# Kernel tuning notes

Hardware: AMD Instinct MI355X
Metric: run time of the kernel (lower is better)

## Reference

```python
import jax, jax.numpy as jnp
import numpy as np

N, E, IN_DIM, H, D = 100000, 1600000, 128, 4, 32


def setup_inputs() -> dict:
    key = jax.random.key(0)
    ks = jax.random.split(key, 8)
    glorot = lambda k, shape: jax.random.uniform(
        k, shape, jnp.float32, -1.0, 1.0) * np.sqrt(6.0 / (shape[0] + shape[1]))
    return {
        "x": jax.random.normal(ks[0], (N, IN_DIM), jnp.float32),
        "row": jax.random.randint(ks[1], (E,), 0, N, jnp.int32),
        "col": jax.random.randint(ks[2], (E,), 0, N, jnp.int32),
        "W_l": glorot(ks[3], (IN_DIM, H * D)),
        "W_r": glorot(ks[4], (IN_DIM, H * D)),
        "a1w": glorot(ks[5], (IN_DIM, H)),
        "a2w": glorot(ks[6], (IN_DIM, H)),
        "bias": jnp.zeros((H * D,), jnp.float32),
    }


def reference(x, row, col, W_l, W_r, a1w, a2w, bias):
    n = x.shape[0]  # num_nodes (= graph[0].max()+1 with dense random rows)
    x_l = (x @ W_l).reshape(n, H, D)          # [N,H,D]
    x_r = x @ W_r                              # [N,H*D]
    # per-edge attention logits: a1[row] + a2[col], leaky-relu(0.2)
    attn = jax.nn.leaky_relu((x @ a1w)[row] + (x @ a2w)[col], 0.2)  # [E,H]
    # segment softmax over destination rows (numerically stable)
    m = jax.ops.segment_max(attn, row, num_segments=n)               # [N,H]
    e = jnp.exp(attn - m[row])
    s = jax.ops.segment_sum(e, row, num_segments=n)                  # [N,H]
    attn_d = e / s[row]                                              # [E,H]
    # per-head SpMM: scatter-add weighted source features to destinations
    msgs = attn_d[:, :, None] * x_l[col]                             # [E,H,D]
    out = jax.ops.segment_sum(msgs, row, num_segments=n).reshape(n, H * D)
    return out + x_r + bias
```

## Files before the change

### kernel.cpp

```cpp
#include <hip/hip_runtime.h>


typedef short bfvec8 __attribute__((ext_vector_type(8)));
typedef float f32x4  __attribute__((ext_vector_type(4)));

#define BK 128
#define CAPC 3584
#define EPB 2048
#define REC 256
#define BSTR 16

__device__ __forceinline__ unsigned short f2bf(float f) {
  union { float f; unsigned int i; } v; v.f = f;
  unsigned int r = v.i + 0x7fffu + ((v.i >> 16) & 1u);
  return (unsigned short)(r >> 16);
}

__global__ __launch_bounds__(128) void wprep_k(
    const float* __restrict__ Wl, const float* __restrict__ Wr,
    const float* __restrict__ a1w, const float* __restrict__ a2w,
    unsigned short* __restrict__ Wtg, int* __restrict__ bcur, int NBK)
{
  const int n = blockIdx.x;
  const int y = blockIdx.y;
  const int k = threadIdx.x;
  if (y == 0 && n < 8) {
    int b = n * 128 + k;
    if (b < NBK) bcur[b * BSTR] = b * CAPC;
  }
  const float* W = y ? Wr : Wl;
  const float LOG2E = 1.4426950408889634f;
  float v;
  if (n < 128)      v = W[(size_t)k * 128 + n];
  else if (y)       v = 0.f;
  else if (n < 132) v = a1w[k * 4 + (n - 128)] * LOG2E;
  else              v = a2w[k * 4 + (n - 132)] * LOG2E;
  Wtg[((size_t)y * 136 + n) * 128 + k] = f2bf(v);
}

__global__ __launch_bounds__(256) void gemm_bin_k(
    const float* __restrict__ x, const unsigned short* __restrict__ Wtg,
    const float* __restrict__ bias,
    char* __restrict__ xls, float* __restrict__ out,
    float* __restrict__ s1, float* __restrict__ s2, int N,
    const int* __restrict__ row, const int* __restrict__ col,
    int* __restrict__ bcur, unsigned int* __restrict__ binned,
    int E, int NBK, int binBlocks, int gemmBlocks)
{
  __shared__ int h[1024];
  __shared__ int base[1024];
  const int bid = blockIdx.x;
  const int t = threadIdx.x;
  const bool isbin = (bid % 3 == 0) && (bid / 3 < binBlocks);

  if (isbin) {
    const int sub = bid / 3;
    const int e0 = sub * EPB;
    const int e1 = min(e0 + EPB, E);

    int rloc[8];
    for (int i = t; i < NBK; i += 256) h[i] = 0;
    __syncthreads();
    #pragma unroll
    for (int k = 0; k < 8; ++k) {
      int e = e0 + t + (k << 8);
      rloc[k] = (e < e1) ? row[e] : -1;
      if (rloc[k] >= 0) atomicAdd(&h[rloc[k] >> 7], 1);
    }
    __syncthreads();
    for (int i = t; i < NBK; i += 256) {
      int c = h[i];
      base[i] = c ? atomicAdd(&bcur[i * BSTR], c) : 0;
    }
    __syncthreads();
    for (int i = t; i < NBK; i += 256) h[i] = 0;
    __syncthreads();
    #pragma unroll
    for (int k = 0; k < 8; ++k) {
      int e = e0 + t + (k << 8);
      if (e < e1) {
        int r = rloc[k];
        unsigned c = (unsigned)col[e];
        int b = r >> 7;
        int rk = atomicAdd(&h[b], 1);
        binned[base[b] + rk] = ((unsigned)(r & 127) << 17) | c;
      }
    }
    return;
  }

  const int sub = bid - min(bid / 3 + 1, binBlocks);
  if (sub >= gemmBlocks) return;
  const int n0 = sub * 64;

  const int w    = t >> 6;
  const int lane = t & 63;
  const int m    = lane & 15;
  const int quad = lane >> 4;
  const int nrow = n0 + 16 * w + m;
  const int kb   = quad * 8;

  bfvec8 afx[4];
  #pragma unroll
  for (int kc4 = 0; kc4 < 4; ++kc4) {
    f32x4 u = (f32x4){0.f, 0.f, 0.f, 0.f};
    f32x4 v = (f32x4){0.f, 0.f, 0.f, 0.f};
    if (nrow < N) {
      const float* xp = &x[(size_t)nrow * 128 + kc4 * 32 + kb];
      u = *(const f32x4*)xp;
      v = *(const f32x4*)(xp + 4);
    }
    bfvec8 a;
    a[0] = (short)f2bf(u[0]); a[1] = (short)f2bf(u[1]);
    a[2] = (short)f2bf(u[2]); a[3] = (short)f2bf(u[3]);
    a[4] = (short)f2bf(v[0]); a[5] = (short)f2bf(v[1]);
    a[6] = (short)f2bf(v[2]); a[7] = (short)f2bf(v[3]);
    afx[kc4] = a;
  }

  const int arow = 128 + (m < 8 ? m : 7);

  #pragma unroll
  for (int y = 0; y < 2; ++y) {
    const unsigned short* Wt = Wtg + (size_t)y * 136 * 128;

    f32x4 acc[9];
    #pragma unroll
    for (int i = 0; i < 9; ++i) acc[i] = (f32x4){0.f, 0.f, 0.f, 0.f};

    #pragma unroll
    for (int kc4 = 0; kc4 < 4; ++kc4) {
      const int kc = kc4 * 32 + kb;
      #pragma unroll
      for (int nt = 0; nt < 8; ++nt) {
        bfvec8 bfr = *(const bfvec8*)&Wt[(size_t)(nt * 16 + m) * 128 + kc];
        acc[nt] = __builtin_amdgcn_mfma_f32_16x16x32_bf16(bfr, afx[kc4], acc[nt], 0, 0, 0);
      }
      if (y == 0) {
        bfvec8 ar = *(const bfvec8*)&Wt[(size_t)arow * 128 + kc];
        acc[8] = __builtin_amdgcn_mfma_f32_16x16x32_bf16(ar, afx[kc4], acc[8], 0, 0, 0);
      }
    }

    if (nrow < N) {
      if (y) {
        #pragma unroll
        for (int nt = 0; nt < 8; ++nt) {
          int c = nt * 16 + quad * 4;
          float4 b4 = *(const float4*)&bias[c];
          float4 v = make_float4(acc[nt][0] + b4.x, acc[nt][1] + b4.y,
                                 acc[nt][2] + b4.z, acc[nt][3] + b4.w);
          *(float4*)&out[(size_t)nrow * 128 + c] = v;
        }
      } else {
        #pragma unroll
        for (int nt = 0; nt < 8; ++nt) {
          int c = nt * 16 + quad * 4;
          unsigned lo = (unsigned)f2bf(acc[nt][0]) | ((unsigned)f2bf(acc[nt][1]) << 16);
          unsigned hi = (unsigned)f2bf(acc[nt][2]) | ((unsigned)f2bf(acc[nt][3]) << 16);
          *(uint2*)(xls + ((size_t)nrow << 8) + 2 * c) = make_uint2(lo, hi);
        }
        if (quad == 0) *(f32x4*)&s1[nrow * 4] = acc[8];
        else if (quad == 1) *(f32x4*)&s2[nrow * 4] = acc[8];
      }
    }
  }
}

__global__ __launch_bounds__(256) void csr_k(const unsigned int* __restrict__ binned,
    const int* __restrict__ bcur, int* __restrict__ offs, int* __restrict__ deg,
    unsigned int* __restrict__ colsort, int N)
{
  __shared__ unsigned ecache[CAPC];
  __shared__ int h[BK];
  __shared__ int sh[BK];
  const int t = threadIdx.x;
  const int b = blockIdx.x;
  const int lo = b * BK;
  const int e0 = b * CAPC;
  const int e1 = bcur[b * BSTR];

  if (t < BK) h[t] = 0;
  __syncthreads();
  for (int i = e0 + t; i < e1; i += 256) {
    unsigned p = binned[i];
    ecache[i - e0] = p;
    atomicAdd(&h[p >> 17], 1);
  }
  __syncthreads();

  int v = 0;
  if (t < BK) { v = h[t]; sh[t] = v; }
  __syncthreads();
  for (int off = 1; off < BK; off <<= 1) {
    int tv = (t < BK && t >= off) ? sh[t - off] : 0;
    __syncthreads();
    if (t < BK) sh[t] += tv;
    __syncthreads();
  }
  if (t < BK) {
    int ex = sh[t] - v;
    int node = lo + t;
    if (node < N) { offs[node] = e0 + ex; deg[node] = v; }
    h[t] = ex;
  }
  __syncthreads();
  const int cnt = e1 - e0;
  for (int i = t; i < cnt; i += 256) {
    unsigned p = ecache[i];
    int rlo = p >> 17;
    unsigned c = p & 0x1FFFFu;
    int pos = atomicAdd(&h[rlo], 1);
    colsort[e0 + pos] = c << 8;
  }
}

__global__ __launch_bounds__(256) void agg_k(const int* __restrict__ offs,
    const int* __restrict__ deg, const unsigned int* __restrict__ colsort,
    const float* __restrict__ s1, const float* __restrict__ s2,
    const char* __restrict__ xls, float* __restrict__ out, int N)
{
  const int lane = threadIdx.x & 63;
  const int n = blockIdx.x * 4 + (threadIdx.x >> 6);
  if (n >= N) return;
  const int e0 = offs[n], e1 = e0 + deg[n];
  const int h  = lane >> 4;
  const int hp = lane & 3;
  const int jj = (lane >> 2) & 7;
  const float s1c = s1[n * 4 + hp];
  const unsigned lane4 = (unsigned)(lane << 2);
  const unsigned hp4   = (unsigned)(hp << 2);
  const char* s2b = (const char*)s2;

  float acc0 = 0.f, acc1 = 0.f, wsum = 0.f;
  int i0 = e0;
  for (; i0 + 8 <= e1; i0 += 8) {
    unsigned csl = colsort[i0 + jj];
    float z2 = *(const float*)(s2b + ((csl >> 4) + hp4));
    float z = s1c + z2;
    z = fmaxf(z, 0.2f * z);
    float wv = exp2f(z);

    unsigned cs[8];
    #pragma unroll
    for (int j = 0; j < 8; ++j) cs[j] = colsort[i0 + j];
    unsigned pv[8];
    #pragma unroll
    for (int j = 0; j < 8; ++j)
      pv[j] = *(const unsigned*)(xls + (cs[j] + lane4));

    #pragma unroll
    for (int j = 0; j < 8; ++j) {
      float wj = __shfl(wv, (j << 2) | h);
      wsum += wj;
      union { unsigned u; float f; } lo, hi;
      lo.u = pv[j] << 16;
      hi.u = pv[j] & 0xffff0000u;
      acc0 += wj * lo.f;
      acc1 += wj * hi.f;
    }
  }
  if (i0 < e1) {
    const int rem = e1 - i0;
    unsigned csl = colsort[i0 + (jj < rem ? jj : rem - 1)];
    float z2 = *(const float*)(s2b + ((csl >> 4) + hp4));
    float z = s1c + z2;
    z = fmaxf(z, 0.2f * z);
    float wv = (jj < rem) ? exp2f(z) : 0.f;

    unsigned cs[8];
    #pragma unroll
    for (int j = 0; j < 8; ++j) cs[j] = colsort[i0 + (j < rem ? j : rem - 1)];
    unsigned pv[8];
    #pragma unroll
    for (int j = 0; j < 8; ++j)
      pv[j] = *(const unsigned*)(xls + (cs[j] + lane4));

    #pragma unroll
    for (int j = 0; j < 8; ++j) {
      float wj = __shfl(wv, (j << 2) | h);
      wsum += wj;
      union { unsigned u; float f; } lo, hi;
      lo.u = pv[j] << 16;
      hi.u = pv[j] & 0xffff0000u;
      acc0 += wj * lo.f;
      acc1 += wj * hi.f;
    }
  }

  float inv = (wsum > 0.f) ? (1.0f / wsum) : 0.f;
  const size_t o = (size_t)n * 128 + 2 * lane;
  float2 xr = *(const float2*)&out[o];
  float2 res; res.x = acc0 * inv + xr.x; res.y = acc1 * inv + xr.y;
  *(float2*)&out[o] = res;
}

extern "C" void kernel_launch(void* const* d_in, const int* in_sizes, int n_in,
                              void* d_out, int out_size, void* d_ws, size_t ws_size,
                              hipStream_t stream) {
  const float* x    = (const float*)d_in[0];
  const int*   row  = (const int*)d_in[1];
  const int*   col  = (const int*)d_in[2];
  const float* Wl   = (const float*)d_in[3];
  const float* Wr   = (const float*)d_in[4];
  const float* a1w  = (const float*)d_in[5];
  const float* a2w  = (const float*)d_in[6];
  const float* bias = (const float*)d_in[7];
  float* out = (float*)d_out;
  const int N = in_sizes[0] / 128;
  const int E = in_sizes[1];
  (void)n_in; (void)out_size; (void)ws_size;

  const int NBK = (N + BK - 1) / BK;

  char* ws = (char*)d_ws;
  size_t off = 0;
  auto carve = [&](size_t bytes) { void* p = ws + off; off += (bytes + 255) & ~(size_t)255; return p; };
  char* xls            = (char*)carve((size_t)N * REC);
  float* s1            = (float*)carve((size_t)N * 4 * 4);
  float* s2            = (float*)carve((size_t)N * 4 * 4);
  int* offs            = (int*)carve((size_t)N * 4);
  int* deg             = (int*)carve((size_t)N * 4);
  unsigned int* colsort= (unsigned int*)carve((size_t)NBK * CAPC * 4);
  unsigned int* binned = (unsigned int*)carve((size_t)NBK * CAPC * 4);
  int* bcur            = (int*)carve((size_t)NBK * BSTR * 4);
  unsigned short* Wtg  = (unsigned short*)carve((size_t)2 * 136 * 128 * 2);

  const int gemmBlocks = (N + 63) / 64;
  const int binBlocks  = (E + EPB - 1) / EPB;
  const int T = gemmBlocks + binBlocks;

  wprep_k   <<<dim3(136, 2), 128, 0, stream>>>(Wl, Wr, a1w, a2w, Wtg, bcur, NBK);
  gemm_bin_k<<<T, 256, 0, stream>>>(x, Wtg, bias, xls, out, s1, s2, N,
                                    row, col, bcur, binned, E, NBK,
                                    binBlocks, gemmBlocks);
  csr_k     <<<NBK, 256, 0, stream>>>(binned, bcur, offs, deg, colsort, N);
  agg_k     <<<(N + 3) / 4, 256, 0, stream>>>(offs, deg, colsort, s1, s2, xls, out, N);
}
```

Measured before the change: 290.5 us.

## Split GEMM blocks per weight matrix, stage weights in LDS, enlarge bin blocks

Each GEMM block now computes only one of the two projections (W_l or W_r), so there are twice as many GEMM blocks. Each block stages its 128x128 bf16 weight tile in shared memory instead of reading it repeatedly from global memory. Edge-binning blocks now handle four times as many edges each, and the interleave ratio between bin and GEMM blocks is computed at launch. csr_k sorts in place in the colsort buffer, which removes the separate binned buffer. In exchange, each GEMM block must load x twice and uses about 34KB of LDS, which may lower occupancy, and each bin block now holds more registers.

```diff
diff --git a/kernel.cpp b/kernel.cpp
--- a/kernel.cpp
+++ b/kernel.cpp
@@ -6,7 +6,7 @@
 
 #define BK 128
 #define CAPC 3584
-#define EPB 2048
+#define EPB 8192
 #define REC 256
 #define BSTR 16
 
@@ -44,25 +44,26 @@
     char* __restrict__ xls, float* __restrict__ out,
     float* __restrict__ s1, float* __restrict__ s2, int N,
     const int* __restrict__ row, const int* __restrict__ col,
-    int* __restrict__ bcur, unsigned int* __restrict__ binned,
-    int E, int NBK, int binBlocks, int gemmBlocks)
+    int* __restrict__ bcur, unsigned int* __restrict__ colsort,
+    int E, int NBK, int binBlocks, int gemmBlocks, int S)
 {
-  __shared__ int h[1024];
-  __shared__ int base[1024];
+  __shared__ __align__(16) char raw[34816];
   const int bid = blockIdx.x;
   const int t = threadIdx.x;
-  const bool isbin = (bid % 3 == 0) && (bid / 3 < binBlocks);
+  const bool isbin = (bid % S == 0) && (bid / S < binBlocks);
 
   if (isbin) {
-    const int sub = bid / 3;
+    int* h    = (int*)raw;
+    int* base = (int*)(raw + 4096);
+    const int sub = bid / S;
     const int e0 = sub * EPB;
     const int e1 = min(e0 + EPB, E);
 
-    int rloc[8];
+    int rloc[32];
     for (int i = t; i < NBK; i += 256) h[i] = 0;
     __syncthreads();
     #pragma unroll
-    for (int k = 0; k < 8; ++k) {
+    for (int k = 0; k < 32; ++k) {
       int e = e0 + t + (k << 8);
       rloc[k] = (e < e1) ? row[e] : -1;
       if (rloc[k] >= 0) atomicAdd(&h[rloc[k] >> 7], 1);
@@ -76,22 +77,30 @@
     for (int i = t; i < NBK; i += 256) h[i] = 0;
     __syncthreads();
     #pragma unroll
-    for (int k = 0; k < 8; ++k) {
+    for (int k = 0; k < 32; ++k) {
       int e = e0 + t + (k << 8);
       if (e < e1) {
         int r = rloc[k];
         unsigned c = (unsigned)col[e];
         int b = r >> 7;
         int rk = atomicAdd(&h[b], 1);
-        binned[base[b] + rk] = ((unsigned)(r & 127) << 17) | c;
+        colsort[base[b] + rk] = ((unsigned)(r & 127) << 17) | c;
       }
     }
     return;
   }
 
-  const int sub = bid - min(bid / 3 + 1, binBlocks);
+  unsigned short (*Ws)[136] = (unsigned short(*)[136])raw;
+  const int sub = bid - min(bid / S + 1, binBlocks);
   if (sub >= gemmBlocks) return;
-  const int n0 = sub * 64;
+  const int y  = sub & 1;
+  const int n0 = (sub >> 1) * 64;
+  const unsigned short* Wt = Wtg + (size_t)y * 136 * 128;
+
+  for (int i = t; i < 2048; i += 256) {
+    int nr = i >> 4, kc = (i & 15) << 3;
+    *(uint4*)&Ws[nr][kc] = *(const uint4*)&Wt[(size_t)nr * 128 + kc];
+  }
 
   const int w    = t >> 6;
   const int lane = t & 63;
@@ -118,56 +127,57 @@
     afx[kc4] = a;
   }
 
-  const int arow = 128 + (m < 8 ? m : 7);
-
+  bfvec8 ar[4];
+  if (y == 0) {
+    int arow = 128 + (m < 8 ? m : 7);
+    #pragma unroll
+    for (int kc4 = 0; kc4 < 4; ++kc4)
+      ar[kc4] = *(const bfvec8*)&Wt[(size_t)arow * 128 + kc4 * 32 + kb];
+  }
+
+  __syncthreads();
+
+  f32x4 acc[9];
   #pragma unroll
-  for (int y = 0; y < 2; ++y) {
-    const unsigned short* Wt = Wtg + (size_t)y * 136 * 128;
-
-    f32x4 acc[9];
-    #pragma unroll
-    for (int i = 0; i < 9; ++i) acc[i] = (f32x4){0.f, 0.f, 0.f, 0.f};
-
-    #pragma unroll
-    for (int kc4 = 0; kc4 < 4; ++kc4) {
-      const int kc = kc4 * 32 + kb;
+  for (int i = 0; i < 9; ++i) acc[i] = (f32x4){0.f, 0.f, 0.f, 0.f};
+
+  #pragma unroll
+  for (int kc4 = 0; kc4 < 4; ++kc4) {
+    const int kc = kc4 * 32 + kb;
+    #pragma unroll
+    for (int nt = 0; nt < 8; ++nt) {
+      bfvec8 bfr = *(const bfvec8*)&Ws[nt * 16 + m][kc];
+      acc[nt] = __builtin_amdgcn_mfma_f32_16x16x32_bf16(bfr, afx[kc4], acc[nt], 0, 0, 0);
+    }
+    if (y == 0)
+      acc[8] = __builtin_amdgcn_mfma_f32_16x16x32_bf16(ar[kc4], afx[kc4], acc[8], 0, 0, 0);
+  }
+
+  if (nrow < N) {
+    if (y) {
       #pragma unroll
       for (int nt = 0; nt < 8; ++nt) {
-        bfvec8 bfr = *(const bfvec8*)&Wt[(size_t)(nt * 16 + m) * 128 + kc];
-        acc[nt] = __builtin_amdgcn_mfma_f32_16x16x32_bf16(bfr, afx[kc4], acc[nt], 0, 0, 0);
+        int c = nt * 16 + quad * 4;
+        float4 b4 = *(const float4*)&bias[c];
+        float4 v = make_float4(acc[nt][0] + b4.x, acc[nt][1] + b4.y,
+                               acc[nt][2] + b4.z, acc[nt][3] + b4.w);
+        *(float4*)&out[(size_t)nrow * 128 + c] = v;
       }
-      if (y == 0) {
-        bfvec8 ar = *(const bfvec8*)&Wt[(size_t)arow * 128 + kc];
-        acc[8] = __builtin_amdgcn_mfma_f32_16x16x32_bf16(ar, afx[kc4], acc[8], 0, 0, 0);
+    } else {
+      #pragma unroll
+      for (int nt = 0; nt < 8; ++nt) {
+        int c = nt * 16 + quad * 4;
+        unsigned lo = (unsigned)f2bf(acc[nt][0]) | ((unsigned)f2bf(acc[nt][1]) << 16);
+        unsigned hi = (unsigned)f2bf(acc[nt][2]) | ((unsigned)f2bf(acc[nt][3]) << 16);
+        *(uint2*)(xls + ((size_t)nrow << 8) + 2 * c) = make_uint2(lo, hi);
       }
-    }
-
-    if (nrow < N) {
-      if (y) {
-        #pragma unroll
-        for (int nt = 0; nt < 8; ++nt) {
-          int c = nt * 16 + quad * 4;
-          float4 b4 = *(const float4*)&bias[c];
-          float4 v = make_float4(acc[nt][0] + b4.x, acc[nt][1] + b4.y,
-                                 acc[nt][2] + b4.z, acc[nt][3] + b4.w);
-          *(float4*)&out[(size_t)nrow * 128 + c] = v;
-        }
-      } else {
-        #pragma unroll
-        for (int nt = 0; nt < 8; ++nt) {
-          int c = nt * 16 + quad * 4;
-          unsigned lo = (unsigned)f2bf(acc[nt][0]) | ((unsigned)f2bf(acc[nt][1]) << 16);
-          unsigned hi = (unsigned)f2bf(acc[nt][2]) | ((unsigned)f2bf(acc[nt][3]) << 16);
-          *(uint2*)(xls + ((size_t)nrow << 8) + 2 * c) = make_uint2(lo, hi);
-        }
-        if (quad == 0) *(f32x4*)&s1[nrow * 4] = acc[8];
-        else if (quad == 1) *(f32x4*)&s2[nrow * 4] = acc[8];
-      }
-    }
-  }
-}
-
-__global__ __launch_bounds__(256) void csr_k(const unsigned int* __restrict__ binned,
+      if (quad == 0) *(f32x4*)&s1[nrow * 4] = acc[8];
+      else if (quad == 1) *(f32x4*)&s2[nrow * 4] = acc[8];
+    }
+  }
+}
+
+__global__ __launch_bounds__(256) void csr_k(
     const int* __restrict__ bcur, int* __restrict__ offs, int* __restrict__ deg,
     unsigned int* __restrict__ colsort, int N)
 {
@@ -183,7 +193,7 @@
   if (t < BK) h[t] = 0;
   __syncthreads();
   for (int i = e0 + t; i < e1; i += 256) {
-    unsigned p = binned[i];
+    unsigned p = colsort[i];
     ecache[i - e0] = p;
     atomicAdd(&h[p >> 17], 1);
   }
@@ -322,18 +332,19 @@
   int* offs            = (int*)carve((size_t)N * 4);
   int* deg             = (int*)carve((size_t)N * 4);
   unsigned int* colsort= (unsigned int*)carve((size_t)NBK * CAPC * 4);
-  unsigned int* binned = (unsigned int*)carve((size_t)NBK * CAPC * 4);
   int* bcur            = (int*)carve((size_t)NBK * BSTR * 4);
   unsigned short* Wtg  = (unsigned short*)carve((size_t)2 * 136 * 128 * 2);
 
-  const int gemmBlocks = (N + 63) / 64;
+  const int nb64       = (N + 63) / 64;
+  const int gemmBlocks = 2 * nb64;
   const int binBlocks  = (E + EPB - 1) / EPB;
-  const int T = gemmBlocks + binBlocks;
+  const int S          = gemmBlocks / binBlocks + 1;
+  const int T          = gemmBlocks + binBlocks;
 
   wprep_k   <<<dim3(136, 2), 128, 0, stream>>>(Wl, Wr, a1w, a2w, Wtg, bcur, NBK);
   gemm_bin_k<<<T, 256, 0, stream>>>(x, Wtg, bias, xls, out, s1, s2, N,
-                                    row, col, bcur, binned, E, NBK,
-                                    binBlocks, gemmBlocks);
-  csr_k     <<<NBK, 256, 0, stream>>>(binned, bcur, offs, deg, colsort, N);
+                                    row, col, bcur, colsort, E, NBK,
+                                    binBlocks, gemmBlocks, S);
+  csr_k     <<<NBK, 256, 0, stream>>>(bcur, offs, deg, colsort, N);
   agg_k     <<<(N + 3) / 4, 256, 0, stream>>>(offs, deg, colsort, s1, s2, xls, out, N);
 }
```

Measured after the change: 445.6 us. +53.4%, slower.
